# Kernel optimization log

Hardware: AMD Instinct MI355X
Metric: run time of the kernel (lower is better)

Reference implementation:

```python
import jax, jax.numpy as jnp
import numpy as np

DIM = 512
NUM_HEADS = 8
HEAD_DIM = DIM // NUM_HEADS
SCALE = HEAD_DIM ** -0.5


def setup_inputs() -> dict:
    key = jax.random.key(0)
    k1, k2, k3, k4 = jax.random.split(key, 4)
    B, C, H, W = 2, DIM, 64, 64
    x = jax.random.normal(k1, (B, C, H, W), dtype=jnp.float32)
    # torch Linear weights are [out, in]; init ~ U(-1/sqrt(in), 1/sqrt(in))
    lim = 1.0 / np.sqrt(C)
    w_qkv = jax.random.uniform(k2, (3 * C, C), minval=-lim, maxval=lim, dtype=jnp.float32)
    w_proj = jax.random.uniform(k3, (C, C), minval=-lim, maxval=lim, dtype=jnp.float32)
    b_proj = jax.random.uniform(k4, (C,), minval=-lim, maxval=lim, dtype=jnp.float32)
    return {"x": x, "w_qkv": w_qkv, "w_proj": w_proj, "b_proj": b_proj}


def reference(x, w_qkv, w_proj, b_proj):
    B, C, H, W = x.shape
    N = H * W
    h, hd = NUM_HEADS, C // NUM_HEADS
    # (B,C,H,W) -> (B,N,C)
    tokens = jnp.transpose(x, (0, 2, 3, 1)).reshape(B, N, C)
    qkv = tokens @ w_qkv.T                              # (B,N,3C)
    qkv = qkv.reshape(B, N, 3, h, hd)
    qkv = jnp.transpose(qkv, (2, 0, 3, 1, 4))           # (3,B,h,N,hd)
    q, k, v = qkv[0], qkv[1], qkv[2]
    k = k * SCALE
    # role-swapped attention: softmax over (k v^T) then apply to q
    attn = jax.nn.softmax(jnp.einsum('bhnd,bhmd->bhnm', k, v), axis=-1)  # (B,h,N,N)
    out = jnp.einsum('bhnm,bhmd->bhnd', attn, q)        # (B,h,N,hd)
    out = jnp.transpose(out, (0, 2, 1, 3)).reshape(B, H, W, C)
    # faithful to original: permute back to (B,C,H,W) THEN reshape to (B,N,C)
    out = jnp.transpose(out, (0, 3, 1, 2)).reshape(B, N, C)
    out = out @ w_proj.T + b_proj
    return out.reshape(B, C, H, W)
```

## Files before the change

### kernel.cpp

```cpp
#include <hip/hip_runtime.h>
#include <hip/hip_bf16.h>
#include <cstdint>


typedef __bf16 bf16_t;
typedef __bf16 bf16x8 __attribute__((ext_vector_type(8)));
typedef float f32x4 __attribute__((ext_vector_type(4)));
typedef unsigned int u32x4 __attribute__((ext_vector_type(4)));

#define DEVFN static __device__ __forceinline__
#define LOG2E 1.4426950408889634f

DEVFN f32x4 mfma16(bf16x8 a, bf16x8 b, f32x4 c) {
  return __builtin_amdgcn_mfma_f32_16x16x32_bf16(a, b, c, 0, 0, 0);
}
DEVFN unsigned bfbits(float x) { return (unsigned)__builtin_bit_cast(unsigned short, (bf16_t)x); }
DEVFN unsigned pack2(float lo, float hi) { return bfbits(lo) | (bfbits(hi) << 16); }

__global__ __launch_bounds__(256) void k_transpose_x(const float* __restrict__ x,
                                                     bf16_t* __restrict__ xT) {
  __shared__ bf16_t tile[64][72];
  int bid = blockIdx.x;
  int ntile = bid & 63;
  int ctile = (bid >> 6) & 7;
  int b = bid >> 9;
  int n0 = ntile << 6, c0 = ctile << 6;
  int t = threadIdx.x;
  int ci = t >> 2, nc = (t & 3) << 4;
  const float4* src4 = reinterpret_cast<const float4*>(
      x + (size_t)(b * 512 + c0 + ci) * 4096 + n0 + nc);
#pragma unroll
  for (int j4 = 0; j4 < 4; ++j4) {
    float4 v = src4[j4];
    tile[ci][nc + j4 * 4 + 0] = (bf16_t)v.x;
    tile[ci][nc + j4 * 4 + 1] = (bf16_t)v.y;
    tile[ci][nc + j4 * 4 + 2] = (bf16_t)v.z;
    tile[ci][nc + j4 * 4 + 3] = (bf16_t)v.w;
  }
  __syncthreads();
  int ni = t & 63, cc = (t >> 6) << 4;
  unsigned ob[8];
#pragma unroll
  for (int j = 0; j < 8; ++j) {
    unsigned lo = (unsigned)__builtin_bit_cast(unsigned short, tile[cc + 2 * j][ni]);
    unsigned hi = (unsigned)__builtin_bit_cast(unsigned short, tile[cc + 2 * j + 1][ni]);
    ob[j] = lo | (hi << 16);
  }
  bf16_t* dst = xT + (size_t)(b * 4096 + n0 + ni) * 512 + c0 + cc;
  reinterpret_cast<u32x4*>(dst)[0] = *(u32x4*)&ob[0];
  reinterpret_cast<u32x4*>(dst)[1] = *(u32x4*)&ob[4];
}

__global__ __launch_bounds__(256) void k_convert_w(const float* __restrict__ w,
                                                   bf16_t* __restrict__ o, int do_scale) {
  int i = (blockIdx.x * 256 + threadIdx.x) * 4;
  float4 v = *reinterpret_cast<const float4*>(w + i);
  if (do_scale) {
    const float s = 0.125f * LOG2E;
    int m = i >> 9;
    if (m >= 512 && m < 1024) { v.x *= s; v.y *= s; v.z *= s; v.w *= s; }
  }
  uint2 st; st.x = pack2(v.x, v.y); st.y = pack2(v.z, v.w);
  *reinterpret_cast<uint2*>(o + i) = st;
}

__global__ __launch_bounds__(256) void k_qkv_gemm(const bf16_t* __restrict__ xT,
                                                  const bf16_t* __restrict__ wq,
                                                  bf16_t* __restrict__ Qn,
                                                  bf16_t* __restrict__ Katt,
                                                  bf16_t* __restrict__ Vbuf) {
  int bid = blockIdx.x;
  int tm = bid / 12, tn = bid % 12;
  int wave = threadIdx.x >> 6, lane = threadIdx.x & 63;
  int n15 = lane & 15, g = lane >> 4;
  int wm = wave & 1, wn = wave >> 1;
  int row0 = tm * 128 + wm * 64;
  int col0 = tn * 128 + wn * 64;
  f32x4 acc[4][4] = {};
  const bf16_t* Ab = xT + (size_t)(row0 + n15) * 512 + g * 8;
  const bf16_t* Bb = wq + (size_t)(col0 + n15) * 512 + g * 8;
  for (int k = 0; k < 512; k += 32) {
    bf16x8 a[4], b[4];
#pragma unroll
    for (int mf = 0; mf < 4; ++mf) a[mf] = *reinterpret_cast<const bf16x8*>(Ab + mf * 16 * 512 + k);
#pragma unroll
    for (int nf = 0; nf < 4; ++nf) b[nf] = *reinterpret_cast<const bf16x8*>(Bb + nf * 16 * 512 + k);
#pragma unroll
    for (int mf = 0; mf < 4; ++mf)
#pragma unroll
      for (int nf = 0; nf < 4; ++nf) acc[mf][nf] = mfma16(a[mf], b[nf], acc[mf][nf]);
  }
  int t = col0 >> 9;
  bf16_t* dstbuf = (t == 0) ? Qn : (t == 1) ? Katt : Vbuf;
#pragma unroll
  for (int mf = 0; mf < 4; ++mf)
#pragma unroll
    for (int r = 0; r < 4; ++r) {
      int rgl = row0 + mf * 16 + g * 4 + r;
      int b_ = rgl >> 12, n = rgl & 4095;
#pragma unroll
      for (int nf = 0; nf < 4; ++nf) {
        int col = col0 + nf * 16 + n15;
        int h = (col >> 6) & 7, d = col & 63;
        dstbuf[(((size_t)(b_ * 8 + h) * 4096 + n) << 6) + d] = (bf16_t)acc[mf][nf][r];
      }
    }
}

__global__ __launch_bounds__(256) void k_transpose_q(const bf16_t* __restrict__ Qn,
                                                     bf16_t* __restrict__ QT) {
  __shared__ bf16_t tile[64][72];
  int bid = blockIdx.x;
  int head = bid >> 6;
  int ntile = bid & 63;
  int n0 = ntile << 6;
  int t = threadIdx.x;
  int i = t >> 2, dc = (t & 3) << 4;
  const bf16_t* src = Qn + ((size_t)head * 4096 + n0 + i) * 64 + dc;
  *(u32x4*)&tile[i][dc] = reinterpret_cast<const u32x4*>(src)[0];
  *(u32x4*)&tile[i][dc + 8] = reinterpret_cast<const u32x4*>(src)[1];
  __syncthreads();
  int d = t & 63, nc2 = (t >> 6) << 4;
  unsigned ob[8];
#pragma unroll
  for (int j = 0; j < 8; ++j) {
    unsigned lo = (unsigned)__builtin_bit_cast(unsigned short, tile[nc2 + 2 * j][d]);
    unsigned hi = (unsigned)__builtin_bit_cast(unsigned short, tile[nc2 + 2 * j + 1][d]);
    ob[j] = lo | (hi << 16);
  }
  bf16_t* dst = QT + ((size_t)head * 64 + d) * 4096 + n0 + nc2;
  reinterpret_cast<u32x4*>(dst)[0] = *(u32x4*)&ob[0];
  reinterpret_cast<u32x4*>(dst)[1] = *(u32x4*)&ob[4];
}

__global__ __launch_bounds__(512, 4) void k_attn(const bf16_t* __restrict__ Katt,
                                                 const bf16_t* __restrict__ Vbuf,
                                                 const bf16_t* __restrict__ QT,
                                                 bf16_t* __restrict__ OT) {
  __shared__ bf16_t Vt[2][4096];
  __shared__ bf16_t Qs[2][4096];
  __shared__ bf16_t tlds[8][16][72];
  int bid = blockIdx.x;
  int head = bid & 15;
  int ntile = bid >> 4;
  int tid = threadIdx.x;
  int wave = tid >> 6, lane = tid & 63;
  int n15 = lane & 15, g = lane >> 4;
  int nrow0 = ntile * 128 + wave * 16;

  const bf16_t* Kp = Katt + ((size_t)head * 4096 + nrow0 + n15) * 64 + g * 8;
  bf16x8 kf0 = *reinterpret_cast<const bf16x8*>(Kp);
  bf16x8 kf1 = *reinterpret_cast<const bf16x8*>(Kp + 32);

  int vrow = tid >> 3, vg = tid & 7;
  int soff = vrow * 64 + ((vg ^ (vrow & 7)) << 3);
  const bf16_t* VgB = Vbuf + ((size_t)head * 4096 + vrow) * 64 + vg * 8;
  const bf16_t* QgB = QT + ((size_t)head * 64 + vrow) * 4096 + vg * 8;

  u32x4 vreg = *reinterpret_cast<const u32x4*>(VgB);
  u32x4 qreg = *reinterpret_cast<const u32x4*>(QgB);
  *reinterpret_cast<u32x4*>(&Vt[0][soff]) = vreg;
  *reinterpret_cast<u32x4*>(&Qs[0][soff]) = qreg;
  __syncthreads();

  f32x4 o[4] = {};
  float lacc = 0.f;
  bool hi_g = (g >= 2);
  int srcA = n15 + 16 * ((2 * g) & 3);
  int srcB = n15 + 16 * ((2 * g + 1) & 3);
  int sw = n15 & 7;
  int voff0 = n15 * 64 + (((g) ^ sw) << 3);
  int voff1 = n15 * 64 + (((g + 4) ^ sw) << 3);

  int cur = 0;
  for (int it = 0; it < 64; ++it) {
    if (it < 63) {
      vreg = *reinterpret_cast<const u32x4*>(VgB + (size_t)(it + 1) * 4096);
      qreg = *reinterpret_cast<const u32x4*>(QgB + (it + 1) * 64);
    }
    const bf16_t* Vl = Vt[cur];
    const bf16_t* Ql = Qs[cur];
    f32x4 p[4];
#pragma unroll
    for (int f = 0; f < 4; ++f) {
      bf16x8 av0 = *reinterpret_cast<const bf16x8*>(Vl + f * 1024 + voff0);
      bf16x8 av1 = *reinterpret_cast<const bf16x8*>(Vl + f * 1024 + voff1);
      f32x4 s = {};
      s = mfma16(av0, kf0, s);
      s = mfma16(av1, kf1, s);
      p[f] = s;
    }
    unsigned pk[4][2];
#pragma unroll
    for (int f = 0; f < 4; ++f) {
#pragma unroll
      for (int r = 0; r < 4; ++r) {
        float e = __builtin_amdgcn_exp2f(p[f][r]);
        p[f][r] = e;
        lacc += e;
      }
      pk[f][0] = pack2(p[f][0], p[f][1]);
      pk[f][1] = pack2(p[f][2], p[f][3]);
    }
    bf16x8 aP[2];
#pragma unroll
    for (int kk = 0; kk < 2; ++kk) {
      unsigned t00a = (unsigned)__shfl((int)pk[2 * kk + 0][0], srcA);
      unsigned t01a = (unsigned)__shfl((int)pk[2 * kk + 0][1], srcA);
      unsigned t10a = (unsigned)__shfl((int)pk[2 * kk + 1][0], srcA);
      unsigned t11a = (unsigned)__shfl((int)pk[2 * kk + 1][1], srcA);
      unsigned t00b = (unsigned)__shfl((int)pk[2 * kk + 0][0], srcB);
      unsigned t01b = (unsigned)__shfl((int)pk[2 * kk + 0][1], srcB);
      unsigned t10b = (unsigned)__shfl((int)pk[2 * kk + 1][0], srcB);
      unsigned t11b = (unsigned)__shfl((int)pk[2 * kk + 1][1], srcB);
      u32x4 uu;
      uu[0] = hi_g ? t10a : t00a;
      uu[1] = hi_g ? t11a : t01a;
      uu[2] = hi_g ? t10b : t00b;
      uu[3] = hi_g ? t11b : t01b;
      aP[kk] = __builtin_bit_cast(bf16x8, uu);
    }
#pragma unroll
    for (int db = 0; db < 4; ++db) {
      bf16x8 bq0 = *reinterpret_cast<const bf16x8*>(Ql + db * 1024 + voff0);
      bf16x8 bq1 = *reinterpret_cast<const bf16x8*>(Ql + db * 1024 + voff1);
      o[db] = mfma16(aP[0], bq0, o[db]);
      o[db] = mfma16(aP[1], bq1, o[db]);
    }
    if (it < 63) {
      *reinterpret_cast<u32x4*>(&Vt[cur ^ 1][soff]) = vreg;
      *reinterpret_cast<u32x4*>(&Qs[cur ^ 1][soff]) = qreg;
    }
    __syncthreads();
    cur ^= 1;
  }

  lacc += __shfl_xor(lacc, 16);
  lacc += __shfl_xor(lacc, 32);
#pragma unroll
  for (int r = 0; r < 4; ++r) {
    float l_r = __shfl(lacc, (g << 2) | r);
    float inv = 1.0f / l_r;
#pragma unroll
    for (int db = 0; db < 4; ++db)
      tlds[wave][g * 4 + r][n15 + 16 * db] = (bf16_t)(o[db][r] * inv);
  }
  __syncthreads();
  {
    int d = lane;
    unsigned ob[8];
#pragma unroll
    for (int j = 0; j < 8; ++j) {
      unsigned lo = (unsigned)__builtin_bit_cast(unsigned short, tlds[wave][2 * j][d]);
      unsigned hi = (unsigned)__builtin_bit_cast(unsigned short, tlds[wave][2 * j + 1][d]);
      ob[j] = lo | (hi << 16);
    }
    bf16_t* dst = OT + ((size_t)head * 64 + d) * 4096 + (size_t)ntile * 128 + wave * 16;
    reinterpret_cast<u32x4*>(dst)[0] = *(u32x4*)&ob[0];
    reinterpret_cast<u32x4*>(dst)[1] = *(u32x4*)&ob[4];
  }
}

__global__ __launch_bounds__(256) void k_proj_gemm(const bf16_t* __restrict__ Y,
                                                   const bf16_t* __restrict__ wp,
                                                   const float* __restrict__ bp,
                                                   float* __restrict__ out) {
  int bid = blockIdx.x;
  int tm = bid >> 2, tn = bid & 3;
  int wave = threadIdx.x >> 6, lane = threadIdx.x & 63;
  int n15 = lane & 15, g = lane >> 4;
  int wm = wave & 1, wn = wave >> 1;
  int row0 = tm * 128 + wm * 64;
  int col0 = tn * 128 + wn * 64;
  f32x4 acc[4][4] = {};
  const bf16_t* Ab = Y + (size_t)(row0 + n15) * 512 + g * 8;
  const bf16_t* Bb = wp + (size_t)(col0 + n15) * 512 + g * 8;
  for (int k = 0; k < 512; k += 32) {
    bf16x8 a[4], b[4];
#pragma unroll
    for (int mf = 0; mf < 4; ++mf) a[mf] = *reinterpret_cast<const bf16x8*>(Ab + mf * 16 * 512 + k);
#pragma unroll
    for (int nf = 0; nf < 4; ++nf) b[nf] = *reinterpret_cast<const bf16x8*>(Bb + nf * 16 * 512 + k);
#pragma unroll
    for (int mf = 0; mf < 4; ++mf)
#pragma unroll
      for (int nf = 0; nf < 4; ++nf) acc[mf][nf] = mfma16(a[mf], b[nf], acc[mf][nf]);
  }
  float bias[4];
#pragma unroll
  for (int nf = 0; nf < 4; ++nf) bias[nf] = bp[col0 + nf * 16 + n15];
#pragma unroll
  for (int mf = 0; mf < 4; ++mf)
#pragma unroll
    for (int r = 0; r < 4; ++r) {
      int rgl = row0 + mf * 16 + g * 4 + r;
#pragma unroll
      for (int nf = 0; nf < 4; ++nf) {
        int col = col0 + nf * 16 + n15;
        out[(size_t)rgl * 512 + col] = acc[mf][nf][r] + bias[nf];
      }
    }
}

extern "C" void kernel_launch(void* const* d_in, const int* in_sizes, int n_in,
                              void* d_out, int out_size, void* d_ws, size_t ws_size,
                              hipStream_t stream) {
  const float* x      = (const float*)d_in[0];
  const float* w_qkv  = (const float*)d_in[1];
  const float* w_proj = (const float*)d_in[2];
  const float* b_proj = (const float*)d_in[3];
  float* out = (float*)d_out;
  char* ws = (char*)d_ws;

  bf16_t* xT    = (bf16_t*)(ws + 0);
  bf16_t* wqkv  = (bf16_t*)(ws + 8388608);
  bf16_t* wproj = (bf16_t*)(ws + 9961472);
  bf16_t* Qn    = (bf16_t*)(ws + 10485760);
  bf16_t* Katt  = (bf16_t*)(ws + 18874368);
  bf16_t* Vbuf  = (bf16_t*)(ws + 27262976);
  bf16_t* QT    = (bf16_t*)(ws + 0);
  bf16_t* OT    = (bf16_t*)(ws + 10485760);

  k_transpose_x<<<dim3(1024), dim3(256), 0, stream>>>(x, xT);
  k_convert_w<<<dim3(768), dim3(256), 0, stream>>>(w_qkv, wqkv, 1);
  k_convert_w<<<dim3(256), dim3(256), 0, stream>>>(w_proj, wproj, 0);
  k_qkv_gemm<<<dim3(768), dim3(256), 0, stream>>>(xT, wqkv, Qn, Katt, Vbuf);
  k_transpose_q<<<dim3(1024), dim3(256), 0, stream>>>(Qn, QT);
  k_attn<<<dim3(512), dim3(512), 0, stream>>>(Katt, Vbuf, QT, OT);
  k_proj_gemm<<<dim3(256), dim3(256), 0, stream>>>(OT, wproj, b_proj, out);
}
```

Measured before the change: 265.5 us.

## Stage QKV and projection GEMM tiles through swizzled double-buffered LDS

Both GEMM kernels now load 128x64 A and B tiles cooperatively into XOR-swizzled shared memory with double buffering and a register prefetch of the next k-slice. They use 512 threads (8 waves), each computing a 64x32 sub-tile. Before, each wave read fragments straight from global memory with redundant loads. The goal is less global traffic and latency overlapped with MFMA work, at the cost of 64KB of LDS per block and a barrier on every step.

```diff
diff --git a/kernel.cpp b/kernel.cpp
--- a/kernel.cpp
+++ b/kernel.cpp
@@ -64,31 +64,75 @@
   *reinterpret_cast<uint2*>(o + i) = st;
 }
 
-__global__ __launch_bounds__(256) void k_qkv_gemm(const bf16_t* __restrict__ xT,
-                                                  const bf16_t* __restrict__ wq,
-                                                  bf16_t* __restrict__ Qn,
-                                                  bf16_t* __restrict__ Katt,
-                                                  bf16_t* __restrict__ Vbuf) {
+__global__ __launch_bounds__(512, 4) void k_qkv_gemm(const bf16_t* __restrict__ xT,
+                                                     const bf16_t* __restrict__ wq,
+                                                     bf16_t* __restrict__ Qn,
+                                                     bf16_t* __restrict__ Katt,
+                                                     bf16_t* __restrict__ Vbuf) {
+  __shared__ bf16_t As[2][128 * 64];
+  __shared__ bf16_t Bs[2][128 * 64];
   int bid = blockIdx.x;
   int tm = bid / 12, tn = bid % 12;
-  int wave = threadIdx.x >> 6, lane = threadIdx.x & 63;
+  int tid = threadIdx.x;
+  int lane = tid & 63, wave = tid >> 6;
   int n15 = lane & 15, g = lane >> 4;
   int wm = wave & 1, wn = wave >> 1;
-  int row0 = tm * 128 + wm * 64;
-  int col0 = tn * 128 + wn * 64;
-  f32x4 acc[4][4] = {};
-  const bf16_t* Ab = xT + (size_t)(row0 + n15) * 512 + g * 8;
-  const bf16_t* Bb = wq + (size_t)(col0 + n15) * 512 + g * 8;
-  for (int k = 0; k < 512; k += 32) {
-    bf16x8 a[4], b[4];
-#pragma unroll
-    for (int mf = 0; mf < 4; ++mf) a[mf] = *reinterpret_cast<const bf16x8*>(Ab + mf * 16 * 512 + k);
-#pragma unroll
-    for (int nf = 0; nf < 4; ++nf) b[nf] = *reinterpret_cast<const bf16x8*>(Bb + nf * 16 * 512 + k);
-#pragma unroll
-    for (int mf = 0; mf < 4; ++mf)
-#pragma unroll
-      for (int nf = 0; nf < 4; ++nf) acc[mf][nf] = mfma16(a[mf], b[nf], acc[mf][nf]);
+  int row0 = tm * 128, col0 = tn * 128;
+
+  int srow = tid >> 3, sslot = tid & 7;
+  int sgran = sslot ^ (srow & 7);
+  const bf16_t* Ag = xT + (size_t)(row0 + srow) * 512 + sgran * 8;
+  const bf16_t* Bg = wq + (size_t)(col0 + srow) * 512 + sgran * 8;
+  int sdst = srow * 64 + sslot * 8;
+
+  u32x4 ra0 = *reinterpret_cast<const u32x4*>(Ag);
+  u32x4 ra1 = *reinterpret_cast<const u32x4*>(Ag + 64 * 512);
+  u32x4 rb0 = *reinterpret_cast<const u32x4*>(Bg);
+  u32x4 rb1 = *reinterpret_cast<const u32x4*>(Bg + 64 * 512);
+  *reinterpret_cast<u32x4*>(&As[0][sdst]) = ra0;
+  *reinterpret_cast<u32x4*>(&As[0][sdst + 4096]) = ra1;
+  *reinterpret_cast<u32x4*>(&Bs[0][sdst]) = rb0;
+  *reinterpret_cast<u32x4*>(&Bs[0][sdst + 4096]) = rb1;
+  __syncthreads();
+
+  f32x4 acc[4][2] = {};
+  int cur = 0;
+  for (int step = 0; step < 8; ++step) {
+    if (step < 7) {
+      int k0n = (step + 1) << 6;
+      ra0 = *reinterpret_cast<const u32x4*>(Ag + k0n);
+      ra1 = *reinterpret_cast<const u32x4*>(Ag + 64 * 512 + k0n);
+      rb0 = *reinterpret_cast<const u32x4*>(Bg + k0n);
+      rb1 = *reinterpret_cast<const u32x4*>(Bg + 64 * 512 + k0n);
+    }
+    const bf16_t* Al = As[cur];
+    const bf16_t* Bl = Bs[cur];
+#pragma unroll
+    for (int kh = 0; kh < 2; ++kh) {
+      bf16x8 a[4], b[2];
+#pragma unroll
+      for (int mf = 0; mf < 4; ++mf) {
+        int r = wm * 64 + mf * 16 + n15;
+        a[mf] = *reinterpret_cast<const bf16x8*>(Al + r * 64 + (((kh * 4 + g) ^ (r & 7)) << 3));
+      }
+#pragma unroll
+      for (int nf = 0; nf < 2; ++nf) {
+        int r = wn * 32 + nf * 16 + n15;
+        b[nf] = *reinterpret_cast<const bf16x8*>(Bl + r * 64 + (((kh * 4 + g) ^ (r & 7)) << 3));
+      }
+#pragma unroll
+      for (int mf = 0; mf < 4; ++mf)
+#pragma unroll
+        for (int nf = 0; nf < 2; ++nf) acc[mf][nf] = mfma16(a[mf], b[nf], acc[mf][nf]);
+    }
+    if (step < 7) {
+      *reinterpret_cast<u32x4*>(&As[cur ^ 1][sdst]) = ra0;
+      *reinterpret_cast<u32x4*>(&As[cur ^ 1][sdst + 4096]) = ra1;
+      *reinterpret_cast<u32x4*>(&Bs[cur ^ 1][sdst]) = rb0;
+      *reinterpret_cast<u32x4*>(&Bs[cur ^ 1][sdst + 4096]) = rb1;
+    }
+    __syncthreads();
+    cur ^= 1;
   }
   int t = col0 >> 9;
   bf16_t* dstbuf = (t == 0) ? Qn : (t == 1) ? Katt : Vbuf;
@@ -96,11 +140,11 @@
   for (int mf = 0; mf < 4; ++mf)
 #pragma unroll
     for (int r = 0; r < 4; ++r) {
-      int rgl = row0 + mf * 16 + g * 4 + r;
+      int rgl = row0 + wm * 64 + mf * 16 + g * 4 + r;
       int b_ = rgl >> 12, n = rgl & 4095;
 #pragma unroll
-      for (int nf = 0; nf < 4; ++nf) {
-        int col = col0 + nf * 16 + n15;
+      for (int nf = 0; nf < 2; ++nf) {
+        int col = col0 + wn * 32 + nf * 16 + n15;
         int h = (col >> 6) & 7, d = col & 63;
         dstbuf[(((size_t)(b_ * 8 + h) * 4096 + n) << 6) + d] = (bf16_t)acc[mf][nf][r];
       }
@@ -261,42 +305,86 @@
   }
 }
 
-__global__ __launch_bounds__(256) void k_proj_gemm(const bf16_t* __restrict__ Y,
-                                                   const bf16_t* __restrict__ wp,
-                                                   const float* __restrict__ bp,
-                                                   float* __restrict__ out) {
+__global__ __launch_bounds__(512, 4) void k_proj_gemm(const bf16_t* __restrict__ Y,
+                                                      const bf16_t* __restrict__ wp,
+                                                      const float* __restrict__ bp,
+                                                      float* __restrict__ out) {
+  __shared__ bf16_t As[2][128 * 64];
+  __shared__ bf16_t Bs[2][128 * 64];
   int bid = blockIdx.x;
   int tm = bid >> 2, tn = bid & 3;
-  int wave = threadIdx.x >> 6, lane = threadIdx.x & 63;
+  int tid = threadIdx.x;
+  int lane = tid & 63, wave = tid >> 6;
   int n15 = lane & 15, g = lane >> 4;
   int wm = wave & 1, wn = wave >> 1;
-  int row0 = tm * 128 + wm * 64;
-  int col0 = tn * 128 + wn * 64;
-  f32x4 acc[4][4] = {};
-  const bf16_t* Ab = Y + (size_t)(row0 + n15) * 512 + g * 8;
-  const bf16_t* Bb = wp + (size_t)(col0 + n15) * 512 + g * 8;
-  for (int k = 0; k < 512; k += 32) {
-    bf16x8 a[4], b[4];
-#pragma unroll
-    for (int mf = 0; mf < 4; ++mf) a[mf] = *reinterpret_cast<const bf16x8*>(Ab + mf * 16 * 512 + k);
-#pragma unroll
-    for (int nf = 0; nf < 4; ++nf) b[nf] = *reinterpret_cast<const bf16x8*>(Bb + nf * 16 * 512 + k);
-#pragma unroll
-    for (int mf = 0; mf < 4; ++mf)
-#pragma unroll
-      for (int nf = 0; nf < 4; ++nf) acc[mf][nf] = mfma16(a[mf], b[nf], acc[mf][nf]);
-  }
-  float bias[4];
-#pragma unroll
-  for (int nf = 0; nf < 4; ++nf) bias[nf] = bp[col0 + nf * 16 + n15];
+  int row0 = tm * 128, col0 = tn * 128;
+
+  int srow = tid >> 3, sslot = tid & 7;
+  int sgran = sslot ^ (srow & 7);
+  const bf16_t* Ag = Y + (size_t)(row0 + srow) * 512 + sgran * 8;
+  const bf16_t* Bg = wp + (size_t)(col0 + srow) * 512 + sgran * 8;
+  int sdst = srow * 64 + sslot * 8;
+
+  u32x4 ra0 = *reinterpret_cast<const u32x4*>(Ag);
+  u32x4 ra1 = *reinterpret_cast<const u32x4*>(Ag + 64 * 512);
+  u32x4 rb0 = *reinterpret_cast<const u32x4*>(Bg);
+  u32x4 rb1 = *reinterpret_cast<const u32x4*>(Bg + 64 * 512);
+  *reinterpret_cast<u32x4*>(&As[0][sdst]) = ra0;
+  *reinterpret_cast<u32x4*>(&As[0][sdst + 4096]) = ra1;
+  *reinterpret_cast<u32x4*>(&Bs[0][sdst]) = rb0;
+  *reinterpret_cast<u32x4*>(&Bs[0][sdst + 4096]) = rb1;
+  __syncthreads();
+
+  f32x4 acc[4][2] = {};
+  int cur = 0;
+  for (int step = 0; step < 8; ++step) {
+    if (step < 7) {
+      int k0n = (step + 1) << 6;
+      ra0 = *reinterpret_cast<const u32x4*>(Ag + k0n);
+      ra1 = *reinterpret_cast<const u32x4*>(Ag + 64 * 512 + k0n);
+      rb0 = *reinterpret_cast<const u32x4*>(Bg + k0n);
+      rb1 = *reinterpret_cast<const u32x4*>(Bg + 64 * 512 + k0n);
+    }
+    const bf16_t* Al = As[cur];
+    const bf16_t* Bl = Bs[cur];
+#pragma unroll
+    for (int kh = 0; kh < 2; ++kh) {
+      bf16x8 a[4], b[2];
+#pragma unroll
+      for (int mf = 0; mf < 4; ++mf) {
+        int r = wm * 64 + mf * 16 + n15;
+        a[mf] = *reinterpret_cast<const bf16x8*>(Al + r * 64 + (((kh * 4 + g) ^ (r & 7)) << 3));
+      }
+#pragma unroll
+      for (int nf = 0; nf < 2; ++nf) {
+        int r = wn * 32 + nf * 16 + n15;
+        b[nf] = *reinterpret_cast<const bf16x8*>(Bl + r * 64 + (((kh * 4 + g) ^ (r & 7)) << 3));
+      }
+#pragma unroll
+      for (int mf = 0; mf < 4; ++mf)
+#pragma unroll
+        for (int nf = 0; nf < 2; ++nf) acc[mf][nf] = mfma16(a[mf], b[nf], acc[mf][nf]);
+    }
+    if (step < 7) {
+      *reinterpret_cast<u32x4*>(&As[cur ^ 1][sdst]) = ra0;
+      *reinterpret_cast<u32x4*>(&As[cur ^ 1][sdst + 4096]) = ra1;
+      *reinterpret_cast<u32x4*>(&Bs[cur ^ 1][sdst]) = rb0;
+      *reinterpret_cast<u32x4*>(&Bs[cur ^ 1][sdst + 4096]) = rb1;
+    }
+    __syncthreads();
+    cur ^= 1;
+  }
+  float bias[2];
+#pragma unroll
+  for (int nf = 0; nf < 2; ++nf) bias[nf] = bp[col0 + wn * 32 + nf * 16 + n15];
 #pragma unroll
   for (int mf = 0; mf < 4; ++mf)
 #pragma unroll
     for (int r = 0; r < 4; ++r) {
-      int rgl = row0 + mf * 16 + g * 4 + r;
-#pragma unroll
-      for (int nf = 0; nf < 4; ++nf) {
-        int col = col0 + nf * 16 + n15;
+      int rgl = row0 + wm * 64 + mf * 16 + g * 4 + r;
+#pragma unroll
+      for (int nf = 0; nf < 2; ++nf) {
+        int col = col0 + wn * 32 + nf * 16 + n15;
         out[(size_t)rgl * 512 + col] = acc[mf][nf][r] + bias[nf];
       }
     }
@@ -324,8 +412,8 @@
   k_transpose_x<<<dim3(1024), dim3(256), 0, stream>>>(x, xT);
   k_convert_w<<<dim3(768), dim3(256), 0, stream>>>(w_qkv, wqkv, 1);
   k_convert_w<<<dim3(256), dim3(256), 0, stream>>>(w_proj, wproj, 0);
-  k_qkv_gemm<<<dim3(768), dim3(256), 0, stream>>>(xT, wqkv, Qn, Katt, Vbuf);
+  k_qkv_gemm<<<dim3(768), dim3(512), 0, stream>>>(xT, wqkv, Qn, Katt, Vbuf);
   k_transpose_q<<<dim3(1024), dim3(256), 0, stream>>>(Qn, QT);
   k_attn<<<dim3(512), dim3(512), 0, stream>>>(Katt, Vbuf, QT, OT);
-  k_proj_gemm<<<dim3(256), dim3(256), 0, stream>>>(OT, wproj, b_proj, out);
-}
+  k_proj_gemm<<<dim3(256), dim3(512), 0, stream>>>(OT, wproj, b_proj, out);
+}
```

After: 239.1 us. -10.0%, faster.
